# Kernel tuning notes

Hardware: AMD Instinct MI355X
Metric: run time of the kernel (lower is better)

The kernel has to match this reference:

```python
import jax, jax.numpy as jnp
import numpy as np

T, B, H, NC, NM = 200, 256, 512, 3, 64  # time, batch, hidden, nb_classes, nb_measures


def setup_inputs() -> dict:
    key = jax.random.key(0)
    ks = jax.random.split(key, 12)

    def p(k, *sh):
        return jax.random.normal(k, sh, dtype=jnp.float32) * 0.05

    return dict(
        cat_seq=jax.random.normal(ks[0], (T, B, NC), dtype=jnp.float32),
        val_seq=jax.random.normal(ks[1], (T, B, NM), dtype=jnp.float32),
        # layer 0 RNN cell: input = nb_classes + nb_measures
        W_ih0=p(ks[2], NC + NM, H), W_hh0=p(ks[3], H, H), b0=p(ks[4], H),
        # layer 1 RNN cell
        W_ih1=p(ks[5], H, H), W_hh1=p(ks[6], H, H), b1=p(ks[7], H),
        # hid2category / hid2measures heads
        Wc=p(ks[8], H, NC), bc=p(ks[9], NC),
        Wm=p(ks[10], H, NM), bm=p(ks[11], NM),
    )


def reference(cat_seq, val_seq, W_ih0, W_hh0, b0, W_ih1, W_hh1, b1, Wc, bc, Wm, bm):
    # Eval mode: dropout masks (i_mask, r_mask) are all ones -> no-ops, omitted.
    batch = val_seq.shape[1]
    h0 = jnp.zeros((batch, W_hh0.shape[0]), dtype=val_seq.dtype)
    h1 = jnp.zeros_like(h0)

    def step(carry, xs):
        h0, h1, cat_i, val_i = carry
        cat_next, val_next = xs
        # predict(): concat(cat, val*i_mask) -> stacked tanh RNN cells -> heads
        x = jnp.concatenate([cat_i, val_i], axis=-1)          # [B, NC+NM]
        h0 = jnp.tanh(x @ W_ih0 + h0 @ W_hh0 + b0)            # [B, H]
        h1 = jnp.tanh(h0 @ W_ih1 + h1 @ W_hh1 + b1)           # [B, H]
        o_cat = jax.nn.softmax(h1 @ Wc + bc, axis=-1)         # [B, NC]
        o_val = h1 @ Wm + bm + val_i                          # [B, NM]
        # impute NaNs of the next timestep with model predictions (on-device)
        val_next = jnp.where(jnp.isnan(val_next), o_val, val_next)
        cat_next = jnp.where(jnp.isnan(cat_next), o_cat, cat_next)
        return (h0, h1, cat_next, val_next), o_cat

    carry0 = (h0, h1, cat_seq[0], val_seq[0])
    _, out_cat = jax.lax.scan(step, carry0, (cat_seq[1:], val_seq[1:]))
    return out_cat  # [T-1, B, NC] == torch.stack(out_cat_seq)
```

## Files before the change

### kernel.cpp

```cpp
#include <hip/hip_runtime.h>
#include <math.h>


#define OFF_H1 131072
#define OFF_Q1 262144
#define OFF_R0 393216
#define OFF_VALC 524288

__device__ __forceinline__ bool nanf_bits(float v) {
  return (__float_as_uint(v) & 0x7fffffffu) > 0x7f800000u;
}

__global__ __launch_bounds__(512) void prologue(
    const float* __restrict__ cat_seq, const float* __restrict__ val_seq,
    const float* __restrict__ Wih0, const float* __restrict__ b0,
    float* __restrict__ h0, float* __restrict__ Q1, float* __restrict__ valc) {
  __shared__ float xs[68];
  const int w = blockIdx.x, tid = threadIdx.x;
  if (tid < 64) {
    float v = val_seq[(size_t)w * 64 + tid];
    valc[(size_t)w * 64 + tid] = v;
    xs[3 + tid] = v;
  } else if (tid < 67) {
    xs[tid - 64] = cat_seq[(size_t)w * 3 + (tid - 64)];
  }
  __syncthreads();
  float a = b0[tid];
  for (int k = 0; k < 67; ++k) a += xs[k] * Wih0[(size_t)k * 512 + tid];
  h0[(size_t)w * 512 + tid] = tanhf(a);
  Q1[(size_t)w * 512 + tid] = 0.f;
}

__global__ __launch_bounds__(256) void s1_kernel(
    const float* __restrict__ h0, const float* __restrict__ Q1,
    const float* __restrict__ Wih1, const float* __restrict__ Whh0,
    const float* __restrict__ b1, float* __restrict__ h1,
    float* __restrict__ R0) {
  __shared__ float smem[16 * 516 + 4 * 576];
  float* As = smem;
  float* red = smem + 16 * 516;
  const int tid = threadIdx.x;
  const int ct = blockIdx.x;
  const int row0 = blockIdx.y * 16;
  const bool isH1 = ct < 16;
  const float* __restrict__ W = isH1 ? Wih1 : Whh0;
  const int cb = (isH1 ? ct : ct - 16) * 32;

  for (int idx = tid; idx < 2048; idx += 256) {
    const int r = idx >> 7, k4 = idx & 127;
    *(float4*)&As[r * 516 + k4 * 4] =
        *(const float4*)&h0[(size_t)(row0 + r) * 512 + k4 * 4];
  }
  __syncthreads();

  const int kq = tid >> 6, rp = (tid >> 3) & 7, cq = tid & 7;
  const int r0 = rp * 2;
  const int kb = kq * 128;
  const float* Wp = W + (size_t)kb * 512 + cb + cq * 4;
  const float* A0 = &As[r0 * 516 + kb];
  const float* A1 = A0 + 516;
  float4 acc0 = {0.f, 0.f, 0.f, 0.f}, acc1 = {0.f, 0.f, 0.f, 0.f};
  for (int k = 0; k < 128; k += 4) {
    const float4 a0 = *(const float4*)(A0 + k);
    const float4 a1 = *(const float4*)(A1 + k);
    const float* wk = Wp + (size_t)k * 512;
    const float4 w0 = *(const float4*)(wk);
    const float4 w1 = *(const float4*)(wk + 512);
    const float4 w2 = *(const float4*)(wk + 1024);
    const float4 w3 = *(const float4*)(wk + 1536);
    acc0.x += a0.x * w0.x + a0.y * w1.x + a0.z * w2.x + a0.w * w3.x;
    acc0.y += a0.x * w0.y + a0.y * w1.y + a0.z * w2.y + a0.w * w3.y;
    acc0.z += a0.x * w0.z + a0.y * w1.z + a0.z * w2.z + a0.w * w3.z;
    acc0.w += a0.x * w0.w + a0.y * w1.w + a0.z * w2.w + a0.w * w3.w;
    acc1.x += a1.x * w0.x + a1.y * w1.x + a1.z * w2.x + a1.w * w3.x;
    acc1.y += a1.x * w0.y + a1.y * w1.y + a1.z * w2.y + a1.w * w3.y;
    acc1.z += a1.x * w0.z + a1.y * w1.z + a1.z * w2.z + a1.w * w3.z;
    acc1.w += a1.x * w0.w + a1.y * w1.w + a1.z * w2.w + a1.w * w3.w;
  }
  {
    float* rw = &red[kq * 576 + r0 * 36 + cq * 4];
    *(float4*)rw = acc0;
    *(float4*)(rw + 36) = acc1;
  }
  __syncthreads();
  {
    const int o = tid * 2;
    const int rr = o >> 5, cc = o & 31;
    const float* rb = &red[rr * 36 + cc];
    const float sx = rb[0] + rb[576] + rb[1152] + rb[1728];
    const float sy = rb[1] + rb[577] + rb[1153] + rb[1729];
    const int col = cb + cc;
    if (isH1) {
      const float2 qv = *(const float2*)&Q1[(size_t)(row0 + rr) * 512 + col];
      float2 o2;
      o2.x = tanhf(sx + qv.x + b1[col]);
      o2.y = tanhf(sy + qv.y + b1[col + 1]);
      *(float2*)&h1[(size_t)(row0 + rr) * 512 + col] = o2;
    } else {
      float2 o2 = {sx, sy};
      *(float2*)&R0[(size_t)(row0 + rr) * 512 + col] = o2;
    }
  }
}

__global__ __launch_bounds__(256) void s2_kernel(
    const float* __restrict__ h1, const float* __restrict__ R0,
    const float* __restrict__ Wih0, const float* __restrict__ b0,
    const float* __restrict__ Whh1, const float* __restrict__ Wc,
    const float* __restrict__ bc, const float* __restrict__ Wm,
    const float* __restrict__ bm, const float* __restrict__ cat_seq,
    const float* __restrict__ val_seq, float* __restrict__ h0,
    float* __restrict__ Q1, float* __restrict__ valc, float* __restrict__ out,
    int t) {
  __shared__ float smem[16 * 516 + 4 * 576];
  const int tid = threadIdx.x;
  if (blockIdx.x < 256) {
    float* As = smem;
    float* red = smem + 16 * 516;
    const int rt = blockIdx.x >> 4, ct = blockIdx.x & 15;
    const int row0 = rt * 16, cb = ct * 32;
    for (int idx = tid; idx < 2048; idx += 256) {
      const int r = idx >> 7, k4 = idx & 127;
      *(float4*)&As[r * 516 + k4 * 4] =
          *(const float4*)&h1[(size_t)(row0 + r) * 512 + k4 * 4];
    }
    __syncthreads();
    const int kq = tid >> 6, rp = (tid >> 3) & 7, cq = tid & 7;
    const int r0 = rp * 2;
    const int kb = kq * 128;
    const float* Wp = Whh1 + (size_t)kb * 512 + cb + cq * 4;
    const float* A0 = &As[r0 * 516 + kb];
    const float* A1 = A0 + 516;
    float4 acc0 = {0.f, 0.f, 0.f, 0.f}, acc1 = {0.f, 0.f, 0.f, 0.f};
    for (int k = 0; k < 128; k += 4) {
      const float4 a0 = *(const float4*)(A0 + k);
      const float4 a1 = *(const float4*)(A1 + k);
      const float* wk = Wp + (size_t)k * 512;
      const float4 w0 = *(const float4*)(wk);
      const float4 w1 = *(const float4*)(wk + 512);
      const float4 w2 = *(const float4*)(wk + 1024);
      const float4 w3 = *(const float4*)(wk + 1536);
      acc0.x += a0.x * w0.x + a0.y * w1.x + a0.z * w2.x + a0.w * w3.x;
      acc0.y += a0.x * w0.y + a0.y * w1.y + a0.z * w2.y + a0.w * w3.y;
      acc0.z += a0.x * w0.z + a0.y * w1.z + a0.z * w2.z + a0.w * w3.z;
      acc0.w += a0.x * w0.w + a0.y * w1.w + a0.z * w2.w + a0.w * w3.w;
      acc1.x += a1.x * w0.x + a1.y * w1.x + a1.z * w2.x + a1.w * w3.x;
      acc1.y += a1.x * w0.y + a1.y * w1.y + a1.z * w2.y + a1.w * w3.y;
      acc1.z += a1.x * w0.z + a1.y * w1.z + a1.z * w2.z + a1.w * w3.z;
      acc1.w += a1.x * w0.w + a1.y * w1.w + a1.z * w2.w + a1.w * w3.w;
    }
    {
      float* rw = &red[kq * 576 + r0 * 36 + cq * 4];
      *(float4*)rw = acc0;
      *(float4*)(rw + 36) = acc1;
    }
    __syncthreads();
    {
      const int o = tid * 2;
      const int rr = o >> 5, cc = o & 31;
      const float* rb = &red[rr * 36 + cc];
      float2 o2;
      o2.x = rb[0] + rb[576] + rb[1152] + rb[1728];
      o2.y = rb[1] + rb[577] + rb[1153] + rb[1729];
      *(float2*)&Q1[(size_t)(row0 + rr) * 512 + cb + cc] = o2;
    }
  } else {
    float* hs = smem;
    float* xsr = smem + 2064;
    float* red2 = smem + 2336;
    float* lg = smem + 3360;
    const int row0 = (blockIdx.x - 256) * 4;
    for (int idx = tid; idx < 512; idx += 256) {
      const int r = idx >> 7, k4 = idx & 127;
      *(float4*)&hs[r * 516 + k4 * 4] =
          *(const float4*)&h1[(size_t)(row0 + r) * 512 + k4 * 4];
    }
    __syncthreads();
    {
      const int ks = tid >> 6, r = (tid >> 4) & 3, qc = tid & 15;
      const int kb = ks * 128;
      const float* hp = &hs[r * 516 + kb];
      const float* wp = Wm + (size_t)kb * 64 + qc * 4;
      float4 a = {0.f, 0.f, 0.f, 0.f};
      for (int k = 0; k < 128; k += 4) {
        const float4 hv = *(const float4*)(hp + k);
        const float* w = wp + (size_t)k * 64;
        const float4 w0 = *(const float4*)(w);
        const float4 w1 = *(const float4*)(w + 64);
        const float4 w2 = *(const float4*)(w + 128);
        const float4 w3 = *(const float4*)(w + 192);
        a.x += hv.x * w0.x + hv.y * w1.x + hv.z * w2.x + hv.w * w3.x;
        a.y += hv.x * w0.y + hv.y * w1.y + hv.z * w2.y + hv.w * w3.y;
        a.z += hv.x * w0.z + hv.y * w1.z + hv.z * w2.z + hv.w * w3.z;
        a.w += hv.x * w0.w + hv.y * w1.w + hv.z * w2.w + hv.w * w3.w;
      }
      *(float4*)&red2[ks * 256 + r * 64 + qc * 4] = a;
    }
    __syncthreads();
    {
      const int r = tid >> 6, m = tid & 63;
      const float s = red2[r * 64 + m] + red2[256 + r * 64 + m] +
                      red2[512 + r * 64 + m] + red2[768 + r * 64 + m];
      const float ov = s + bm[m] + valc[(size_t)(row0 + r) * 64 + m];
      const float raw =
          val_seq[(size_t)(t + 1) * 16384 + (size_t)(row0 + r) * 64 + m];
      const float nv = nanf_bits(raw) ? ov : raw;
      valc[(size_t)(row0 + r) * 64 + m] = nv;
      xsr[r * 68 + 3 + m] = nv;
    }
    {
      const int r = tid >> 6, lane = tid & 63;
      float a0 = 0.f, a1 = 0.f, a2 = 0.f;
      const float* hp = &hs[r * 516 + lane * 8];
      const float* wp = Wc + (size_t)lane * 24;
#pragma unroll
      for (int kk = 0; kk < 8; ++kk) {
        const float h = hp[kk];
        a0 += h * wp[kk * 3 + 0];
        a1 += h * wp[kk * 3 + 1];
        a2 += h * wp[kk * 3 + 2];
      }
#pragma unroll
      for (int off = 32; off >= 1; off >>= 1) {
        a0 += __shfl_down(a0, off);
        a1 += __shfl_down(a1, off);
        a2 += __shfl_down(a2, off);
      }
      if (lane == 0) {
        lg[r * 3 + 0] = a0 + bc[0];
        lg[r * 3 + 1] = a1 + bc[1];
        lg[r * 3 + 2] = a2 + bc[2];
      }
    }
    __syncthreads();
    if (tid < 4) {
      const int r = tid;
      const float l0 = lg[r * 3], l1 = lg[r * 3 + 1], l2 = lg[r * 3 + 2];
      const float mx = fmaxf(l0, fmaxf(l1, l2));
      const float e0 = expf(l0 - mx), e1 = expf(l1 - mx), e2 = expf(l2 - mx);
      const float inv = 1.f / (e0 + e1 + e2);
      const float p0 = e0 * inv, p1 = e1 * inv, p2 = e2 * inv;
      const size_t ob = (size_t)t * 768 + (size_t)(row0 + r) * 3;
      out[ob] = p0; out[ob + 1] = p1; out[ob + 2] = p2;
      const size_t cbx = (size_t)(t + 1) * 768 + (size_t)(row0 + r) * 3;
      const float c0 = cat_seq[cbx], c1 = cat_seq[cbx + 1],
                  c2 = cat_seq[cbx + 2];
      xsr[r * 68 + 0] = nanf_bits(c0) ? p0 : c0;
      xsr[r * 68 + 1] = nanf_bits(c1) ? p1 : c1;
      xsr[r * 68 + 2] = nanf_bits(c2) ? p2 : c2;
    }
    __syncthreads();
    {
      const int c4 = (tid & 127) * 4;
      const int rh = tid >> 7;
#pragma unroll
      for (int rw = 0; rw < 2; ++rw) {
        const int r = rh * 2 + rw;
        float4 acc = *(const float4*)&R0[(size_t)(row0 + r) * 512 + c4];
        const float4 bv = *(const float4*)&b0[c4];
        acc.x += bv.x; acc.y += bv.y; acc.z += bv.z; acc.w += bv.w;
        for (int k = 0; k < 67; ++k) {
          const float x = xsr[r * 68 + k];
          const float4 w = *(const float4*)&Wih0[(size_t)k * 512 + c4];
          acc.x += x * w.x; acc.y += x * w.y;
          acc.z += x * w.z; acc.w += x * w.w;
        }
        float4 o4;
        o4.x = tanhf(acc.x); o4.y = tanhf(acc.y);
        o4.z = tanhf(acc.z); o4.w = tanhf(acc.w);
        *(float4*)&h0[(size_t)(row0 + r) * 512 + c4] = o4;
      }
    }
  }
}

extern "C" void kernel_launch(void* const* d_in, const int* in_sizes, int n_in,
                              void* d_out, int out_size, void* d_ws, size_t ws_size,
                              hipStream_t stream) {
  const float* cat_seq = (const float*)d_in[0];
  const float* val_seq = (const float*)d_in[1];
  const float* Wih0 = (const float*)d_in[2];
  const float* Whh0 = (const float*)d_in[3];
  const float* b0 = (const float*)d_in[4];
  const float* Wih1 = (const float*)d_in[5];
  const float* Whh1 = (const float*)d_in[6];
  const float* b1 = (const float*)d_in[7];
  const float* Wc = (const float*)d_in[8];
  const float* bc = (const float*)d_in[9];
  const float* Wm = (const float*)d_in[10];
  const float* bm = (const float*)d_in[11];
  float* ws = (float*)d_ws;
  float* h0 = ws;
  float* h1 = ws + OFF_H1;
  float* Q1 = ws + OFF_Q1;
  float* R0 = ws + OFF_R0;
  float* valc = ws + OFF_VALC;
  float* out = (float*)d_out;

  hipLaunchKernelGGL(prologue, dim3(256), dim3(512), 0, stream,
                     cat_seq, val_seq, Wih0, b0, h0, Q1, valc);
  for (int t = 0; t < 199; ++t) {
    hipLaunchKernelGGL(s1_kernel, dim3(32, 16), dim3(256), 0, stream,
                       h0, Q1, Wih1, Whh0, b1, h1, R0);
    hipLaunchKernelGGL(s2_kernel, dim3(320), dim3(256), 0, stream,
                       h1, R0, Wih0, b0, Whh1, Wc, bc, Wm, bm,
                       cat_seq, val_seq, h0, Q1, valc, out, t);
  }
}
```

Measured before the change: 6.034 ms.

## Pack recurrent weights into column tiles and double threads per block

A one-time kernel repacks Wih1/Whh0/Whh1 into contiguous 32-column tiles, so each block streams a compact 64KB tile instead of strided rows of a 512-wide matrix. Both step kernels move to 512 threads with an 8-way split-K and an 8-way reduction, and grid ordering changes so consecutive blocks share a weight tile. The goal is better cache-line use and more latency hiding per block. In exchange it adds a pack launch, more workspace, and larger shared-memory reductions.

```diff
diff --git a/kernel.cpp b/kernel.cpp
--- a/kernel.cpp
+++ b/kernel.cpp
@@ -6,9 +6,28 @@
 #define OFF_Q1 262144
 #define OFF_R0 393216
 #define OFF_VALC 524288
+#define OFF_WP1 540672
+#define OFF_WP2 1064960
 
 __device__ __forceinline__ bool nanf_bits(float v) {
   return (__float_as_uint(v) & 0x7fffffffu) > 0x7f800000u;
+}
+
+__global__ __launch_bounds__(256) void pack_weights(
+    const float* __restrict__ Wih1, const float* __restrict__ Whh0,
+    const float* __restrict__ Whh1, float* __restrict__ WP1,
+    float* __restrict__ WP2) {
+  const unsigned idx0 = blockIdx.x * 256u + threadIdx.x;
+  const unsigned stride = gridDim.x * 256u;
+  for (unsigned i = idx0; i < 524288u; i += stride) {
+    const unsigned ct = i >> 14, rem = i & 16383u, k = rem >> 5, c = rem & 31u;
+    WP1[i] = (ct < 16u) ? Wih1[k * 512u + ct * 32u + c]
+                        : Whh0[k * 512u + (ct - 16u) * 32u + c];
+  }
+  for (unsigned i = idx0; i < 262144u; i += stride) {
+    const unsigned ct = i >> 14, rem = i & 16383u, k = rem >> 5, c = rem & 31u;
+    WP2[i] = Whh1[k * 512u + ct * 32u + c];
+  }
 }
 
 __global__ __launch_bounds__(512) void prologue(
@@ -31,43 +50,32 @@
   Q1[(size_t)w * 512 + tid] = 0.f;
 }
 
-__global__ __launch_bounds__(256) void s1_kernel(
-    const float* __restrict__ h0, const float* __restrict__ Q1,
-    const float* __restrict__ Wih1, const float* __restrict__ Whh0,
-    const float* __restrict__ b1, float* __restrict__ h1,
-    float* __restrict__ R0) {
-  __shared__ float smem[16 * 516 + 4 * 576];
-  float* As = smem;
-  float* red = smem + 16 * 516;
-  const int tid = threadIdx.x;
-  const int ct = blockIdx.x;
-  const int row0 = blockIdx.y * 16;
-  const bool isH1 = ct < 16;
-  const float* __restrict__ W = isH1 ? Wih1 : Whh0;
-  const int cb = (isH1 ? ct : ct - 16) * 32;
-
-  for (int idx = tid; idx < 2048; idx += 256) {
+__device__ __forceinline__ void gemm_tile_16x32(
+    const float* __restrict__ Arows, const float* __restrict__ Wtile,
+    float* __restrict__ As, float* __restrict__ red, const int tid,
+    const int row0) {
+  for (int idx = tid; idx < 2048; idx += 512) {
     const int r = idx >> 7, k4 = idx & 127;
     *(float4*)&As[r * 516 + k4 * 4] =
-        *(const float4*)&h0[(size_t)(row0 + r) * 512 + k4 * 4];
+        *(const float4*)&Arows[(size_t)(row0 + r) * 512 + k4 * 4];
   }
   __syncthreads();
-
-  const int kq = tid >> 6, rp = (tid >> 3) & 7, cq = tid & 7;
-  const int r0 = rp * 2;
-  const int kb = kq * 128;
-  const float* Wp = W + (size_t)kb * 512 + cb + cq * 4;
+  const int kq = tid >> 6, pos = tid & 63;
+  const int rp = pos >> 3, cq = pos & 7;
+  const int r0 = rp * 2, kb = kq * 64;
+  const float* Wp = Wtile + (size_t)kb * 32 + cq * 4;
   const float* A0 = &As[r0 * 516 + kb];
   const float* A1 = A0 + 516;
   float4 acc0 = {0.f, 0.f, 0.f, 0.f}, acc1 = {0.f, 0.f, 0.f, 0.f};
-  for (int k = 0; k < 128; k += 4) {
+#pragma unroll 4
+  for (int k = 0; k < 64; k += 4) {
     const float4 a0 = *(const float4*)(A0 + k);
     const float4 a1 = *(const float4*)(A1 + k);
-    const float* wk = Wp + (size_t)k * 512;
+    const float* wk = Wp + k * 32;
     const float4 w0 = *(const float4*)(wk);
-    const float4 w1 = *(const float4*)(wk + 512);
-    const float4 w2 = *(const float4*)(wk + 1024);
-    const float4 w3 = *(const float4*)(wk + 1536);
+    const float4 w1 = *(const float4*)(wk + 32);
+    const float4 w2 = *(const float4*)(wk + 64);
+    const float4 w3 = *(const float4*)(wk + 96);
     acc0.x += a0.x * w0.x + a0.y * w1.x + a0.z * w2.x + a0.w * w3.x;
     acc0.y += a0.x * w0.y + a0.y * w1.y + a0.z * w2.y + a0.w * w3.y;
     acc0.z += a0.x * w0.z + a0.y * w1.z + a0.z * w2.z + a0.w * w3.z;
@@ -77,112 +85,84 @@
     acc1.z += a1.x * w0.z + a1.y * w1.z + a1.z * w2.z + a1.w * w3.z;
     acc1.w += a1.x * w0.w + a1.y * w1.w + a1.z * w2.w + a1.w * w3.w;
   }
-  {
-    float* rw = &red[kq * 576 + r0 * 36 + cq * 4];
-    *(float4*)rw = acc0;
-    *(float4*)(rw + 36) = acc1;
-  }
+  float* rw = &red[(kq * 16 + r0) * 36 + cq * 4];
+  *(float4*)rw = acc0;
+  *(float4*)(rw + 36) = acc1;
   __syncthreads();
-  {
-    const int o = tid * 2;
-    const int rr = o >> 5, cc = o & 31;
-    const float* rb = &red[rr * 36 + cc];
-    const float sx = rb[0] + rb[576] + rb[1152] + rb[1728];
-    const float sy = rb[1] + rb[577] + rb[1153] + rb[1729];
-    const int col = cb + cc;
-    if (isH1) {
-      const float2 qv = *(const float2*)&Q1[(size_t)(row0 + rr) * 512 + col];
-      float2 o2;
-      o2.x = tanhf(sx + qv.x + b1[col]);
-      o2.y = tanhf(sy + qv.y + b1[col + 1]);
-      *(float2*)&h1[(size_t)(row0 + rr) * 512 + col] = o2;
-    } else {
-      float2 o2 = {sx, sy};
-      *(float2*)&R0[(size_t)(row0 + rr) * 512 + col] = o2;
-    }
-  }
-}
-
-__global__ __launch_bounds__(256) void s2_kernel(
+}
+
+__global__ __launch_bounds__(512) void s1_kernel(
+    const float* __restrict__ h0, const float* __restrict__ Q1,
+    const float* __restrict__ WP1, const float* __restrict__ b1,
+    float* __restrict__ h1, float* __restrict__ R0) {
+  __shared__ float smem[16 * 516 + 8 * 16 * 36];
+  float* As = smem;
+  float* red = smem + 16 * 516;
+  const int tid = threadIdx.x;
+  const int ct = blockIdx.x >> 4, rt = blockIdx.x & 15;
+  const int row0 = rt * 16;
+  const bool isH1 = ct < 16;
+  const int cb = (isH1 ? ct : ct - 16) * 32;
+
+  gemm_tile_16x32(h0, WP1 + (size_t)ct * 16384, As, red, tid, row0);
+
+  const int rr = tid >> 5, cc = tid & 31;
+  const float* rb = &red[rr * 36 + cc];
+  float s = 0.f;
+#pragma unroll
+  for (int q = 0; q < 8; ++q) s += rb[q * 576];
+  const int row = row0 + rr, col = cb + cc;
+  if (isH1) {
+    h1[(size_t)row * 512 + col] =
+        tanhf(s + Q1[(size_t)row * 512 + col] + b1[col]);
+  } else {
+    R0[(size_t)row * 512 + col] = s;
+  }
+}
+
+__global__ __launch_bounds__(512) void s2_kernel(
     const float* __restrict__ h1, const float* __restrict__ R0,
-    const float* __restrict__ Wih0, const float* __restrict__ b0,
-    const float* __restrict__ Whh1, const float* __restrict__ Wc,
+    const float* __restrict__ WP2, const float* __restrict__ Wih0,
+    const float* __restrict__ b0, const float* __restrict__ Wc,
     const float* __restrict__ bc, const float* __restrict__ Wm,
     const float* __restrict__ bm, const float* __restrict__ cat_seq,
     const float* __restrict__ val_seq, float* __restrict__ h0,
     float* __restrict__ Q1, float* __restrict__ valc, float* __restrict__ out,
     int t) {
-  __shared__ float smem[16 * 516 + 4 * 576];
+  __shared__ float smem[16 * 516 + 8 * 16 * 36];
   const int tid = threadIdx.x;
   if (blockIdx.x < 256) {
     float* As = smem;
     float* red = smem + 16 * 516;
-    const int rt = blockIdx.x >> 4, ct = blockIdx.x & 15;
+    const int ct = blockIdx.x >> 4, rt = blockIdx.x & 15;
     const int row0 = rt * 16, cb = ct * 32;
-    for (int idx = tid; idx < 2048; idx += 256) {
-      const int r = idx >> 7, k4 = idx & 127;
-      *(float4*)&As[r * 516 + k4 * 4] =
-          *(const float4*)&h1[(size_t)(row0 + r) * 512 + k4 * 4];
-    }
-    __syncthreads();
-    const int kq = tid >> 6, rp = (tid >> 3) & 7, cq = tid & 7;
-    const int r0 = rp * 2;
-    const int kb = kq * 128;
-    const float* Wp = Whh1 + (size_t)kb * 512 + cb + cq * 4;
-    const float* A0 = &As[r0 * 516 + kb];
-    const float* A1 = A0 + 516;
-    float4 acc0 = {0.f, 0.f, 0.f, 0.f}, acc1 = {0.f, 0.f, 0.f, 0.f};
-    for (int k = 0; k < 128; k += 4) {
-      const float4 a0 = *(const float4*)(A0 + k);
-      const float4 a1 = *(const float4*)(A1 + k);
-      const float* wk = Wp + (size_t)k * 512;
-      const float4 w0 = *(const float4*)(wk);
-      const float4 w1 = *(const float4*)(wk + 512);
-      const float4 w2 = *(const float4*)(wk + 1024);
-      const float4 w3 = *(const float4*)(wk + 1536);
-      acc0.x += a0.x * w0.x + a0.y * w1.x + a0.z * w2.x + a0.w * w3.x;
-      acc0.y += a0.x * w0.y + a0.y * w1.y + a0.z * w2.y + a0.w * w3.y;
-      acc0.z += a0.x * w0.z + a0.y * w1.z + a0.z * w2.z + a0.w * w3.z;
-      acc0.w += a0.x * w0.w + a0.y * w1.w + a0.z * w2.w + a0.w * w3.w;
-      acc1.x += a1.x * w0.x + a1.y * w1.x + a1.z * w2.x + a1.w * w3.x;
-      acc1.y += a1.x * w0.y + a1.y * w1.y + a1.z * w2.y + a1.w * w3.y;
-      acc1.z += a1.x * w0.z + a1.y * w1.z + a1.z * w2.z + a1.w * w3.z;
-      acc1.w += a1.x * w0.w + a1.y * w1.w + a1.z * w2.w + a1.w * w3.w;
-    }
-    {
-      float* rw = &red[kq * 576 + r0 * 36 + cq * 4];
-      *(float4*)rw = acc0;
-      *(float4*)(rw + 36) = acc1;
-    }
-    __syncthreads();
-    {
-      const int o = tid * 2;
-      const int rr = o >> 5, cc = o & 31;
-      const float* rb = &red[rr * 36 + cc];
-      float2 o2;
-      o2.x = rb[0] + rb[576] + rb[1152] + rb[1728];
-      o2.y = rb[1] + rb[577] + rb[1153] + rb[1729];
-      *(float2*)&Q1[(size_t)(row0 + rr) * 512 + cb + cc] = o2;
-    }
+    gemm_tile_16x32(h1, WP2 + (size_t)ct * 16384, As, red, tid, row0);
+    const int rr = tid >> 5, cc = tid & 31;
+    const float* rb = &red[rr * 36 + cc];
+    float s = 0.f;
+#pragma unroll
+    for (int q = 0; q < 8; ++q) s += rb[q * 576];
+    Q1[(size_t)(row0 + rr) * 512 + cb + cc] = s;
   } else {
     float* hs = smem;
-    float* xsr = smem + 2064;
-    float* red2 = smem + 2336;
-    float* lg = smem + 3360;
+    float* red2 = smem + 2064;
+    float* xsr = smem + 4112;
+    float* lg = smem + 4384;
     const int row0 = (blockIdx.x - 256) * 4;
-    for (int idx = tid; idx < 512; idx += 256) {
-      const int r = idx >> 7, k4 = idx & 127;
+    {
+      const int r = tid >> 7, k4 = tid & 127;
       *(float4*)&hs[r * 516 + k4 * 4] =
           *(const float4*)&h1[(size_t)(row0 + r) * 512 + k4 * 4];
     }
     __syncthreads();
     {
       const int ks = tid >> 6, r = (tid >> 4) & 3, qc = tid & 15;
-      const int kb = ks * 128;
+      const int kb = ks * 64;
       const float* hp = &hs[r * 516 + kb];
       const float* wp = Wm + (size_t)kb * 64 + qc * 4;
       float4 a = {0.f, 0.f, 0.f, 0.f};
-      for (int k = 0; k < 128; k += 4) {
+#pragma unroll 4
+      for (int k = 0; k < 64; k += 4) {
         const float4 hv = *(const float4*)(hp + k);
         const float* w = wp + (size_t)k * 64;
         const float4 w0 = *(const float4*)(w);
@@ -197,19 +177,19 @@
       *(float4*)&red2[ks * 256 + r * 64 + qc * 4] = a;
     }
     __syncthreads();
-    {
+    if (tid < 256) {
       const int r = tid >> 6, m = tid & 63;
-      const float s = red2[r * 64 + m] + red2[256 + r * 64 + m] +
-                      red2[512 + r * 64 + m] + red2[768 + r * 64 + m];
+      float s = 0.f;
+#pragma unroll
+      for (int q = 0; q < 8; ++q) s += red2[q * 256 + r * 64 + m];
       const float ov = s + bm[m] + valc[(size_t)(row0 + r) * 64 + m];
       const float raw =
           val_seq[(size_t)(t + 1) * 16384 + (size_t)(row0 + r) * 64 + m];
       const float nv = nanf_bits(raw) ? ov : raw;
       valc[(size_t)(row0 + r) * 64 + m] = nv;
       xsr[r * 68 + 3 + m] = nv;
-    }
-    {
-      const int r = tid >> 6, lane = tid & 63;
+    } else {
+      const int r = (tid >> 6) - 4, lane = tid & 63;
       float a0 = 0.f, a1 = 0.f, a2 = 0.f;
       const float* hp = &hs[r * 516 + lane * 8];
       const float* wp = Wc + (size_t)lane * 24;
@@ -251,25 +231,20 @@
     }
     __syncthreads();
     {
-      const int c4 = (tid & 127) * 4;
-      const int rh = tid >> 7;
-#pragma unroll
-      for (int rw = 0; rw < 2; ++rw) {
-        const int r = rh * 2 + rw;
-        float4 acc = *(const float4*)&R0[(size_t)(row0 + r) * 512 + c4];
-        const float4 bv = *(const float4*)&b0[c4];
-        acc.x += bv.x; acc.y += bv.y; acc.z += bv.z; acc.w += bv.w;
-        for (int k = 0; k < 67; ++k) {
-          const float x = xsr[r * 68 + k];
-          const float4 w = *(const float4*)&Wih0[(size_t)k * 512 + c4];
-          acc.x += x * w.x; acc.y += x * w.y;
-          acc.z += x * w.z; acc.w += x * w.w;
-        }
-        float4 o4;
-        o4.x = tanhf(acc.x); o4.y = tanhf(acc.y);
-        o4.z = tanhf(acc.z); o4.w = tanhf(acc.w);
-        *(float4*)&h0[(size_t)(row0 + r) * 512 + c4] = o4;
-      }
+      const int r = tid >> 7, c4 = (tid & 127) * 4;
+      float4 acc = *(const float4*)&R0[(size_t)(row0 + r) * 512 + c4];
+      const float4 bv = *(const float4*)&b0[c4];
+      acc.x += bv.x; acc.y += bv.y; acc.z += bv.z; acc.w += bv.w;
+      for (int k = 0; k < 67; ++k) {
+        const float x = xsr[r * 68 + k];
+        const float4 w = *(const float4*)&Wih0[(size_t)k * 512 + c4];
+        acc.x += x * w.x; acc.y += x * w.y;
+        acc.z += x * w.z; acc.w += x * w.w;
+      }
+      float4 o4;
+      o4.x = tanhf(acc.x); o4.y = tanhf(acc.y);
+      o4.z = tanhf(acc.z); o4.w = tanhf(acc.w);
+      *(float4*)&h0[(size_t)(row0 + r) * 512 + c4] = o4;
     }
   }
 }
@@ -295,15 +270,19 @@
   float* Q1 = ws + OFF_Q1;
   float* R0 = ws + OFF_R0;
   float* valc = ws + OFF_VALC;
+  float* WP1 = ws + OFF_WP1;
+  float* WP2 = ws + OFF_WP2;
   float* out = (float*)d_out;
 
+  hipLaunchKernelGGL(pack_weights, dim3(512), dim3(256), 0, stream,
+                     Wih1, Whh0, Whh1, WP1, WP2);
   hipLaunchKernelGGL(prologue, dim3(256), dim3(512), 0, stream,
                      cat_seq, val_seq, Wih0, b0, h0, Q1, valc);
   for (int t = 0; t < 199; ++t) {
-    hipLaunchKernelGGL(s1_kernel, dim3(32, 16), dim3(256), 0, stream,
-                       h0, Q1, Wih1, Whh0, b1, h1, R0);
-    hipLaunchKernelGGL(s2_kernel, dim3(320), dim3(256), 0, stream,
-                       h1, R0, Wih0, b0, Whh1, Wc, bc, Wm, bm,
+    hipLaunchKernelGGL(s1_kernel, dim3(512), dim3(512), 0, stream,
+                       h0, Q1, WP1, b1, h1, R0);
+    hipLaunchKernelGGL(s2_kernel, dim3(320), dim3(512), 0, stream,
+                       h1, R0, WP2, Wih0, b0, Wc, bc, Wm, bm,
                        cat_seq, val_seq, h0, Q1, valc, out, t);
   }
 }
```

Measured after the change: 9.052 ms. +50.0%, slower.
